# Optimization experiments

Hardware: AMD Instinct MI355X
Metric: run time of the kernel (lower is better)

## Reference

```python
import jax, jax.numpy as jnp
import numpy as np

N_NODES = 100000
N_EDGES = 1600000
IN_CH = 64
HID = 128
OUT_CH = 2
N_GRAPHS = 512
LN_EPS = 1e-5


def setup_inputs() -> dict:
    key = jax.random.key(0)
    ks = jax.random.split(key, 16)
    x = jax.random.normal(ks[0], (N_NODES, IN_CH), dtype=jnp.float32)
    edge_index = jax.random.randint(ks[1], (2, N_EDGES), 0, N_NODES, dtype=jnp.int64)
    batch = jnp.sort(jax.random.randint(ks[2], (N_NODES,), 0, N_GRAPHS, dtype=jnp.int64))

    def lin(k, fan_in, fan_out):
        bound = 1.0 / np.sqrt(fan_in)
        return jax.random.uniform(k, (fan_in, fan_out), jnp.float32, -bound, bound)

    inp = {"x": x, "edge_index": edge_index, "batch": batch}
    # SAGEConv 0: in->hid; SAGEConv 1,2: hid->hid
    inp["Wl0"] = lin(ks[3], IN_CH, HID); inp["bl0"] = jnp.zeros((HID,), jnp.float32)
    inp["Wr0"] = lin(ks[4], IN_CH, HID)
    inp["Wl1"] = lin(ks[5], HID, HID); inp["bl1"] = jnp.zeros((HID,), jnp.float32)
    inp["Wr1"] = lin(ks[6], HID, HID)
    inp["Wl2"] = lin(ks[7], HID, HID); inp["bl2"] = jnp.zeros((HID,), jnp.float32)
    inp["Wr2"] = lin(ks[8], HID, HID)
    # decode: LayerNorm(hid) + Linear(hid, out)
    inp["ln_g"] = jnp.ones((HID,), jnp.float32)
    inp["ln_b"] = jnp.zeros((HID,), jnp.float32)
    inp["Wd"] = lin(ks[9], HID, OUT_CH)
    inp["bd"] = jnp.zeros((OUT_CH,), jnp.float32)
    return inp


def _sage_conv(x, src, dst, Wl, bl, Wr):
    # mean aggregation of source features onto destination nodes
    s = jax.ops.segment_sum(x[src], dst, num_segments=N_NODES)  # [N, F]
    cnt = jax.ops.segment_sum(jnp.ones((src.shape[0],), x.dtype), dst, num_segments=N_NODES)
    agg = s / jnp.maximum(cnt, 1.0)[:, None]
    return agg @ Wl + bl + x @ Wr


def reference(x, edge_index, batch, Wl0, bl0, Wr0, Wl1, bl1, Wr1, Wl2, bl2, Wr2, ln_g, ln_b, Wd, bd):
    src, dst = edge_index[0], edge_index[1]
    h = jax.nn.relu(_sage_conv(x, src, dst, Wl0, bl0, Wr0))
    h = jax.nn.relu(_sage_conv(h, src, dst, Wl1, bl1, Wr1))
    h = jax.nn.relu(_sage_conv(h, src, dst, Wl2, bl2, Wr2))
    # global_add_pool
    g = jax.ops.segment_sum(h, batch, num_segments=N_GRAPHS)  # [G, HID]
    # decode: LayerNorm + Linear
    mu = jnp.mean(g, axis=-1, keepdims=True)
    var = jnp.mean(jnp.square(g - mu), axis=-1, keepdims=True)
    gn = (g - mu) * jax.lax.rsqrt(var + LN_EPS) * ln_g + ln_b
    return gn @ Wd + bd
```

## Files before the change

kernel.cpp:

```cpp
#include <hip/hip_runtime.h>

#define N_NODES  100000
#define N_EDGES  1600000
#define N_GRAPHS 512
#define LN_EPS   1e-5f

#define NB    256
#define NPB   391
#define BCAP  8192
#define PCHUNK 8192
#define PBLOCKS ((N_EDGES + PCHUNK - 1) / PCHUNK)
#define POOL_CHUNK 64
#define POOL_BLOCKS ((N_NODES + POOL_CHUNK - 1) / POOL_CHUNK)

typedef unsigned short u16;
typedef unsigned int   u32;
typedef __attribute__((ext_vector_type(8))) short bf16x8;
typedef __attribute__((ext_vector_type(4))) float f32x4;

__device__ __forceinline__ float b2f(u16 v) {
    u32 u = ((u32)v) << 16;
    return __builtin_bit_cast(float, u);
}
__device__ __forceinline__ u16 f2b(float f) {
    u32 u = __builtin_bit_cast(u32, f);
    u32 r = (u + 0x7fffu + ((u >> 16) & 1u)) >> 16;
    return (u16)r;
}


__global__ __launch_bounds__(256)
void partition_edges(const int* __restrict__ src, const int* __restrict__ dst,
                     int* __restrict__ bcnt, uint2* __restrict__ bpool) {
    __shared__ int hist[NB];
    __shared__ int gbase[NB];
    __shared__ int cur[NB];
    int t = threadIdx.x;
    int e0 = blockIdx.x * PCHUNK;
    int e1 = e0 + PCHUNK; if (e1 > N_EDGES) e1 = N_EDGES;

    hist[t] = 0;
    __syncthreads();
    for (int e = e0 + t; e < e1; e += 256)
        atomicAdd(&hist[dst[e] / NPB], 1);
    __syncthreads();
    int h = hist[t];
    gbase[t] = (h > 0) ? atomicAdd(&bcnt[t], h) : 0;
    cur[t] = 0;
    __syncthreads();
    for (int e = e0 + t; e < e1; e += 256) {
        int d = dst[e], s = src[e];
        int b = d / NPB;
        int p = atomicAdd(&cur[b], 1);
        bpool[(size_t)b * BCAP + gbase[b] + p] = make_uint2((u32)d, (u32)s);
    }
}

__global__ void scan_buckets(const int* __restrict__ bcnt, int* __restrict__ bbase,
                             int* __restrict__ offsets) {
    __shared__ int sh[NB];
    int t = threadIdx.x;
    int v = bcnt[t];
    sh[t] = v; __syncthreads();
    for (int off = 1; off < NB; off <<= 1) {
        int add = (t >= off) ? sh[t - off] : 0;
        __syncthreads();
        sh[t] += add;
        __syncthreads();
    }
    bbase[t] = sh[t] - v;
    if (t == NB - 1) offsets[N_NODES] = sh[t];
}

__global__ __launch_bounds__(256)
void build_csr_bucket(const int* __restrict__ bcnt, const int* __restrict__ bbase,
                      const uint2* __restrict__ bpool,
                      int* __restrict__ offsets, int* __restrict__ csr) {
    __shared__ int sA[512];
    __shared__ int sB[512];
    __shared__ int csrL[BCAP];
    int b = blockIdx.x, t = threadIdx.x;
    int nlo = b * NPB;
    int NL = N_NODES - nlo; if (NL > NPB) NL = NPB;
    int count = bcnt[b], base = bbase[b];
    const uint2* pool = bpool + (size_t)b * BCAP;

    sA[t] = 0; sA[t + 256] = 0;
    __syncthreads();
    for (int i = t; i < count; i += 256)
        atomicAdd(&sA[(int)pool[i].x - nlo], 1);
    __syncthreads();
    int c0 = sA[t], c1 = sA[t + 256];

    int* a = sA; int* c = sB;
    for (int off = 1; off < 512; off <<= 1) {
        c[t]       = a[t]       + ((t >= off)       ? a[t - off]       : 0);
        c[t + 256] = a[t + 256] + ((t + 256 >= off) ? a[t + 256 - off] : 0);
        __syncthreads();
        int* tmp = a; a = c; c = tmp;
    }
    int ex0 = a[t] - c0, ex1 = a[t + 256] - c1;
    if (t < NL)       offsets[nlo + t]       = base + ex0;
    if (t + 256 < NL) offsets[nlo + t + 256] = base + ex1;
    c[t] = ex0; c[t + 256] = ex1;
    __syncthreads();
    for (int i = t; i < count; i += 256) {
        uint2 p = pool[i];
        int pos = atomicAdd(&c[(int)p.x - nlo], 1);
        csrL[pos] = (int)p.y;
    }
    __syncthreads();
    for (int i = t; i < count; i += 256)
        csr[base + i] = csrL[i];
}


__global__ __launch_bounds__(256)
void conv_f32_bf16(const float* __restrict__ in, u16* __restrict__ out, int n4) {
    int i = blockIdx.x * 256 + threadIdx.x;
    if (i < n4) {
        float4 v = ((const float4*)in)[i];
        u32 lo = (u32)f2b(v.x) | ((u32)f2b(v.y) << 16);
        u32 hi = (u32)f2b(v.z) | ((u32)f2b(v.w) << 16);
        ((uint2*)out)[i] = make_uint2(lo, hi);
    }
}

__global__ __launch_bounds__(256)
void conv_weights(const float* __restrict__ Wl, const float* __restrict__ Wr,
                  int K1, int KC, u16* __restrict__ Wt) {
    int idx = blockIdx.x * 256 + threadIdx.x;
    if (idx >= 128 * KC) return;
    int c = idx / KC, k = idx % KC;
    float v = (k < K1) ? Wl[k * 128 + c] : Wr[(k - K1) * 128 + c];
    Wt[idx] = f2b(v);
}


template<int F>
__global__ __launch_bounds__(256)
void aggregate_bf16(const u16* __restrict__ in, const int* __restrict__ offsets,
                    const int* __restrict__ csr, u16* __restrict__ out) {
    int grp = threadIdx.x >> 5;
    int sub = threadIdx.x & 31;
    int n = blockIdx.x * 8 + grp;
    int o0 = offsets[n], o1 = offsets[n + 1];
    int d = o1 - o0;
    float inv = 1.0f / (float)(d > 1 ? d : 1);

    if (F == 128) {
        const uint2* base = (const uint2*)in;
        float acc[4][4];
        #pragma unroll
        for (int j = 0; j < 4; j++)
            #pragma unroll
            for (int c = 0; c < 4; c++) acc[j][c] = 0.f;

        int o = o0;
        for (; o + 4 <= o1; o += 4) {
            int s0 = csr[o + 0], s1 = csr[o + 1], s2 = csr[o + 2], s3 = csr[o + 3];
            uint2 v0 = base[(size_t)s0 * 32 + sub];
            uint2 v1 = base[(size_t)s1 * 32 + sub];
            uint2 v2 = base[(size_t)s2 * 32 + sub];
            uint2 v3 = base[(size_t)s3 * 32 + sub];
            acc[0][0] += b2f((u16)(v0.x & 0xffffu)); acc[0][1] += b2f((u16)(v0.x >> 16));
            acc[0][2] += b2f((u16)(v0.y & 0xffffu)); acc[0][3] += b2f((u16)(v0.y >> 16));
            acc[1][0] += b2f((u16)(v1.x & 0xffffu)); acc[1][1] += b2f((u16)(v1.x >> 16));
            acc[1][2] += b2f((u16)(v1.y & 0xffffu)); acc[1][3] += b2f((u16)(v1.y >> 16));
            acc[2][0] += b2f((u16)(v2.x & 0xffffu)); acc[2][1] += b2f((u16)(v2.x >> 16));
            acc[2][2] += b2f((u16)(v2.y & 0xffffu)); acc[2][3] += b2f((u16)(v2.y >> 16));
            acc[3][0] += b2f((u16)(v3.x & 0xffffu)); acc[3][1] += b2f((u16)(v3.x >> 16));
            acc[3][2] += b2f((u16)(v3.y & 0xffffu)); acc[3][3] += b2f((u16)(v3.y >> 16));
        }
        for (; o < o1; o++) {
            int s = csr[o];
            uint2 v = base[(size_t)s * 32 + sub];
            acc[0][0] += b2f((u16)(v.x & 0xffffu)); acc[0][1] += b2f((u16)(v.x >> 16));
            acc[0][2] += b2f((u16)(v.y & 0xffffu)); acc[0][3] += b2f((u16)(v.y >> 16));
        }
        float r0 = ((acc[0][0] + acc[1][0]) + (acc[2][0] + acc[3][0])) * inv;
        float r1 = ((acc[0][1] + acc[1][1]) + (acc[2][1] + acc[3][1])) * inv;
        float r2 = ((acc[0][2] + acc[1][2]) + (acc[2][2] + acc[3][2])) * inv;
        float r3 = ((acc[0][3] + acc[1][3]) + (acc[2][3] + acc[3][3])) * inv;
        uint2 w;
        w.x = (u32)f2b(r0) | ((u32)f2b(r1) << 16);
        w.y = (u32)f2b(r2) | ((u32)f2b(r3) << 16);
        ((uint2*)out)[(size_t)n * 32 + sub] = w;
    } else {
        const u32* base = (const u32*)in;
        float acc[4][2];
        #pragma unroll
        for (int j = 0; j < 4; j++) { acc[j][0] = 0.f; acc[j][1] = 0.f; }

        int o = o0;
        for (; o + 4 <= o1; o += 4) {
            int s0 = csr[o + 0], s1 = csr[o + 1], s2 = csr[o + 2], s3 = csr[o + 3];
            u32 v0 = base[(size_t)s0 * 32 + sub];
            u32 v1 = base[(size_t)s1 * 32 + sub];
            u32 v2 = base[(size_t)s2 * 32 + sub];
            u32 v3 = base[(size_t)s3 * 32 + sub];
            acc[0][0] += b2f((u16)(v0 & 0xffffu)); acc[0][1] += b2f((u16)(v0 >> 16));
            acc[1][0] += b2f((u16)(v1 & 0xffffu)); acc[1][1] += b2f((u16)(v1 >> 16));
            acc[2][0] += b2f((u16)(v2 & 0xffffu)); acc[2][1] += b2f((u16)(v2 >> 16));
            acc[3][0] += b2f((u16)(v3 & 0xffffu)); acc[3][1] += b2f((u16)(v3 >> 16));
        }
        for (; o < o1; o++) {
            int s = csr[o];
            u32 v = base[(size_t)s * 32 + sub];
            acc[0][0] += b2f((u16)(v & 0xffffu)); acc[0][1] += b2f((u16)(v >> 16));
        }
        float r0 = ((acc[0][0] + acc[1][0]) + (acc[2][0] + acc[3][0])) * inv;
        float r1 = ((acc[0][1] + acc[1][1]) + (acc[2][1] + acc[3][1])) * inv;
        ((u32*)out)[(size_t)n * 32 + sub] = (u32)f2b(r0) | ((u32)f2b(r1) << 16);
    }
}


template<int KHALF>
__global__ __launch_bounds__(256)
void gemm_mfma(const u16* __restrict__ A1, const u16* __restrict__ A2,
               const u16* __restrict__ Wt, const float* __restrict__ bias,
               u16* __restrict__ out) {
    constexpr int KC  = 2 * KHALF;
    constexpr int NKS = KC / 32;

    int t = threadIdx.x;
    int lane = t & 63, w = t >> 6;
    int l15 = lane & 15, l4 = lane >> 4;
    int mbase = blockIdx.x * 64;

    bf16x8 bfr[2][NKS];
    #pragma unroll
    for (int ct = 0; ct < 2; ct++)
        #pragma unroll
        for (int ks = 0; ks < NKS; ks++) {
            int row = w * 32 + ct * 16 + l15;
            int kb  = ks * 32 + l4 * 8;
            bfr[ct][ks] = *reinterpret_cast<const bf16x8*>(Wt + row * KC + kb);
        }

    f32x4 acc[4][2];
    #pragma unroll
    for (int i = 0; i < 4; i++)
        #pragma unroll
        for (int j = 0; j < 2; j++)
            acc[i][j] = (f32x4){0.f, 0.f, 0.f, 0.f};

    const bf16x8 zfr = {0, 0, 0, 0, 0, 0, 0, 0};

    #pragma unroll
    for (int ks = 0; ks < NKS; ks++) {
        const u16* Ab = (ks < NKS / 2) ? A1 : A2;
        int kb = (ks < NKS / 2) ? (ks * 32 + l4 * 8) : ((ks - NKS / 2) * 32 + l4 * 8);
        bf16x8 afr[4];
        #pragma unroll
        for (int rt = 0; rt < 4; rt++) {
            int row = mbase + rt * 16 + l15;
            afr[rt] = (row < N_NODES)
                ? *reinterpret_cast<const bf16x8*>(Ab + (size_t)row * KHALF + kb)
                : zfr;
        }
        #pragma unroll
        for (int rt = 0; rt < 4; rt++)
            #pragma unroll
            for (int ct = 0; ct < 2; ct++)
                acc[rt][ct] = __builtin_amdgcn_mfma_f32_16x16x32_bf16(
                    afr[rt], bfr[ct][ks], acc[rt][ct], 0, 0, 0);
    }

    #pragma unroll
    for (int ct = 0; ct < 2; ct++) {
        int col = w * 32 + ct * 16 + l15;
        float bv = bias[col];
        #pragma unroll
        for (int rt = 0; rt < 4; rt++) {
            #pragma unroll
            for (int j = 0; j < 4; j++) {
                int row = mbase + rt * 16 + l4 * 4 + j;
                if (row < N_NODES) {
                    float v = fmaxf(acc[rt][ct][j] + bv, 0.f);
                    out[(size_t)row * 128 + col] = f2b(v);
                }
            }
        }
    }
}


__global__ __launch_bounds__(128)
void pool_partial(const u16* __restrict__ h, const int* __restrict__ batch,
                  float* __restrict__ gpool) {
    int c = threadIdx.x;
    int n0 = blockIdx.x * POOL_CHUNK;
    int n1 = n0 + POOL_CHUNK; if (n1 > N_NODES) n1 = N_NODES;
    float run = 0.f;
    int curg = -1;
    for (int r = n0; r < n1; r++) {
        int gid = batch[r];
        if (gid != curg) {
            if (curg >= 0) atomicAdd(&gpool[curg * 128 + c], run);
            run = 0.f; curg = gid;
        }
        run += b2f(h[(size_t)r * 128 + c]);
    }
    if (curg >= 0) atomicAdd(&gpool[curg * 128 + c], run);
}

__global__ __launch_bounds__(64)
void ln_decode(const float* __restrict__ gpool,
               const float* __restrict__ ln_g, const float* __restrict__ ln_b,
               const float* __restrict__ Wd, const float* __restrict__ bd,
               float* __restrict__ out) {
    int g = blockIdx.x, lane = threadIdx.x;
    float v0 = gpool[g * 128 + lane];
    float v1 = gpool[g * 128 + 64 + lane];
    float s = v0 + v1;
    #pragma unroll
    for (int off = 32; off > 0; off >>= 1) s += __shfl_xor(s, off, 64);
    float mu = s * (1.0f / 128.f);
    float d0 = v0 - mu, d1 = v1 - mu;
    float q = d0 * d0 + d1 * d1;
    #pragma unroll
    for (int off = 32; off > 0; off >>= 1) q += __shfl_xor(q, off, 64);
    float rs = rsqrtf(q * (1.0f / 128.f) + LN_EPS);
    float gn0 = d0 * rs * ln_g[lane]      + ln_b[lane];
    float gn1 = d1 * rs * ln_g[64 + lane] + ln_b[64 + lane];
    float o0 = gn0 * Wd[lane * 2 + 0] + gn1 * Wd[(64 + lane) * 2 + 0];
    float o1 = gn0 * Wd[lane * 2 + 1] + gn1 * Wd[(64 + lane) * 2 + 1];
    #pragma unroll
    for (int off = 32; off > 0; off >>= 1) {
        o0 += __shfl_xor(o0, off, 64);
        o1 += __shfl_xor(o1, off, 64);
    }
    if (lane == 0) {
        out[g * 2 + 0] = o0 + bd[0];
        out[g * 2 + 1] = o1 + bd[1];
    }
}


extern "C" void kernel_launch(void* const* d_in, const int* in_sizes, int n_in,
                              void* d_out, int out_size, void* d_ws, size_t ws_size,
                              hipStream_t stream) {
    (void)in_sizes; (void)n_in; (void)out_size; (void)ws_size;

    const float* x     = (const float*)d_in[0];
    const int*   ei    = (const int*)d_in[1];
    const int*   batch = (const int*)d_in[2];
    const float* Wl0 = (const float*)d_in[3];
    const float* bl0 = (const float*)d_in[4];
    const float* Wr0 = (const float*)d_in[5];
    const float* Wl1 = (const float*)d_in[6];
    const float* bl1 = (const float*)d_in[7];
    const float* Wr1 = (const float*)d_in[8];
    const float* Wl2 = (const float*)d_in[9];
    const float* bl2 = (const float*)d_in[10];
    const float* Wr2 = (const float*)d_in[11];
    const float* ln_g = (const float*)d_in[12];
    const float* ln_b = (const float*)d_in[13];
    const float* Wd  = (const float*)d_in[14];
    const float* bd  = (const float*)d_in[15];
    float* out = (float*)d_out;

    const int* src = ei;
    const int* dst = ei + N_EDGES;

    char* ws = (char*)d_ws;
    int*   csr     = (int*)(ws + 0);
    int*   offsets = (int*)(ws + 6400000);
    int*   bcnt    = (int*)(ws + 6800128);
    int*   bbase   = (int*)(ws + 6801152);
    uint2* bpool   = (uint2*)(ws + 6802176);
    u16*   x16     = (u16*)(ws + 23579392);
    u16*   aggbuf  = (u16*)(ws + 36379392);
    u16*   bufB    = (u16*)(ws + 61979392);
    u16*   bufC    = (u16*)(ws + 87579392);
    u16*   Wt0     = (u16*)(ws + 113179392);
    u16*   Wt1     = (u16*)(ws + 113212160);
    u16*   Wt2     = (u16*)(ws + 113277696);
    float* gpool   = (float*)(ws + 113343232);

    hipMemsetAsync(bcnt, 0, NB * sizeof(int), stream);
    hipMemsetAsync(gpool, 0, N_GRAPHS * 128 * sizeof(float), stream);

    partition_edges<<<PBLOCKS, 256, 0, stream>>>(src, dst, bcnt, bpool);
    scan_buckets<<<1, 256, 0, stream>>>(bcnt, bbase, offsets);
    build_csr_bucket<<<NB, 256, 0, stream>>>(bcnt, bbase, bpool, offsets, csr);

    conv_f32_bf16<<<(N_NODES * 64 / 4 + 255) / 256, 256, 0, stream>>>(x, x16, N_NODES * 64 / 4);
    conv_weights<<<(128 * 128 + 255) / 256, 256, 0, stream>>>(Wl0, Wr0, 64, 128, Wt0);
    conv_weights<<<(128 * 256 + 255) / 256, 256, 0, stream>>>(Wl1, Wr1, 128, 256, Wt1);
    conv_weights<<<(128 * 256 + 255) / 256, 256, 0, stream>>>(Wl2, Wr2, 128, 256, Wt2);

    const int aggGrid  = N_NODES / 8;
    const int gemmGrid = (N_NODES + 63) / 64;

    aggregate_bf16<64><<<aggGrid, 256, 0, stream>>>(x16, offsets, csr, aggbuf);
    gemm_mfma<64><<<gemmGrid, 256, 0, stream>>>(aggbuf, x16, Wt0, bl0, bufB);
    aggregate_bf16<128><<<aggGrid, 256, 0, stream>>>(bufB, offsets, csr, aggbuf);
    gemm_mfma<128><<<gemmGrid, 256, 0, stream>>>(aggbuf, bufB, Wt1, bl1, bufC);
    aggregate_bf16<128><<<aggGrid, 256, 0, stream>>>(bufC, offsets, csr, aggbuf);
    gemm_mfma<128><<<gemmGrid, 256, 0, stream>>>(aggbuf, bufC, Wt2, bl2, bufB);

    pool_partial<<<POOL_BLOCKS, 128, 0, stream>>>(bufB, batch, gpool);
    ln_decode<<<N_GRAPHS, 64, 0, stream>>>(gpool, ln_g, ln_b, Wd, bd, out);
}
```

Measured before the change: 375.4 us.

## Split neighbor aggregation into column slices for better cache locality

Replaces the per-node full-row aggregation kernel with a sliced one. Each block handles 32 nodes but only one 8-u32 (32-byte) column slice of the feature row, with blocks ordered slice-major within each chunk. The aim is to shrink the per-pass working set of gathered rows so random neighbor gathers hit L2/MALL more often. It also adds nontemporal loads for the CSR and nontemporal stores for the output. The cost is that CSR indices and offsets are read once per slice (4x or 8x), each gather moves only 32 bytes per row segment, and there are many more blocks.

```diff
diff --git a/kernel.cpp b/kernel.cpp
--- a/kernel.cpp
+++ b/kernel.cpp
@@ -137,82 +137,48 @@
 }
 
 
-template<int F>
-__global__ __launch_bounds__(256)
-void aggregate_bf16(const u16* __restrict__ in, const int* __restrict__ offsets,
-                    const int* __restrict__ csr, u16* __restrict__ out) {
-    int grp = threadIdx.x >> 5;
-    int sub = threadIdx.x & 31;
-    int n = blockIdx.x * 8 + grp;
+template<int ROWU32, int SLICES>
+__global__ __launch_bounds__(256)
+void aggregate_slice(const u16* __restrict__ in, const int* __restrict__ offsets,
+                     const int* __restrict__ csr, u16* __restrict__ out) {
+    int slice = blockIdx.x & (SLICES - 1);
+    int chunk = blockIdx.x / SLICES;
+    int grp = threadIdx.x >> 3;
+    int sub = threadIdx.x & 7;
+    int n = chunk * 32 + grp;
     int o0 = offsets[n], o1 = offsets[n + 1];
-    int d = o1 - o0;
-    float inv = 1.0f / (float)(d > 1 ? d : 1);
-
-    if (F == 128) {
-        const uint2* base = (const uint2*)in;
-        float acc[4][4];
-        #pragma unroll
-        for (int j = 0; j < 4; j++)
-            #pragma unroll
-            for (int c = 0; c < 4; c++) acc[j][c] = 0.f;
-
-        int o = o0;
-        for (; o + 4 <= o1; o += 4) {
-            int s0 = csr[o + 0], s1 = csr[o + 1], s2 = csr[o + 2], s3 = csr[o + 3];
-            uint2 v0 = base[(size_t)s0 * 32 + sub];
-            uint2 v1 = base[(size_t)s1 * 32 + sub];
-            uint2 v2 = base[(size_t)s2 * 32 + sub];
-            uint2 v3 = base[(size_t)s3 * 32 + sub];
-            acc[0][0] += b2f((u16)(v0.x & 0xffffu)); acc[0][1] += b2f((u16)(v0.x >> 16));
-            acc[0][2] += b2f((u16)(v0.y & 0xffffu)); acc[0][3] += b2f((u16)(v0.y >> 16));
-            acc[1][0] += b2f((u16)(v1.x & 0xffffu)); acc[1][1] += b2f((u16)(v1.x >> 16));
-            acc[1][2] += b2f((u16)(v1.y & 0xffffu)); acc[1][3] += b2f((u16)(v1.y >> 16));
-            acc[2][0] += b2f((u16)(v2.x & 0xffffu)); acc[2][1] += b2f((u16)(v2.x >> 16));
-            acc[2][2] += b2f((u16)(v2.y & 0xffffu)); acc[2][3] += b2f((u16)(v2.y >> 16));
-            acc[3][0] += b2f((u16)(v3.x & 0xffffu)); acc[3][1] += b2f((u16)(v3.x >> 16));
-            acc[3][2] += b2f((u16)(v3.y & 0xffffu)); acc[3][3] += b2f((u16)(v3.y >> 16));
-        }
-        for (; o < o1; o++) {
-            int s = csr[o];
-            uint2 v = base[(size_t)s * 32 + sub];
-            acc[0][0] += b2f((u16)(v.x & 0xffffu)); acc[0][1] += b2f((u16)(v.x >> 16));
-            acc[0][2] += b2f((u16)(v.y & 0xffffu)); acc[0][3] += b2f((u16)(v.y >> 16));
-        }
-        float r0 = ((acc[0][0] + acc[1][0]) + (acc[2][0] + acc[3][0])) * inv;
-        float r1 = ((acc[0][1] + acc[1][1]) + (acc[2][1] + acc[3][1])) * inv;
-        float r2 = ((acc[0][2] + acc[1][2]) + (acc[2][2] + acc[3][2])) * inv;
-        float r3 = ((acc[0][3] + acc[1][3]) + (acc[2][3] + acc[3][3])) * inv;
-        uint2 w;
-        w.x = (u32)f2b(r0) | ((u32)f2b(r1) << 16);
-        w.y = (u32)f2b(r2) | ((u32)f2b(r3) << 16);
-        ((uint2*)out)[(size_t)n * 32 + sub] = w;
-    } else {
-        const u32* base = (const u32*)in;
-        float acc[4][2];
-        #pragma unroll
-        for (int j = 0; j < 4; j++) { acc[j][0] = 0.f; acc[j][1] = 0.f; }
-
-        int o = o0;
-        for (; o + 4 <= o1; o += 4) {
-            int s0 = csr[o + 0], s1 = csr[o + 1], s2 = csr[o + 2], s3 = csr[o + 3];
-            u32 v0 = base[(size_t)s0 * 32 + sub];
-            u32 v1 = base[(size_t)s1 * 32 + sub];
-            u32 v2 = base[(size_t)s2 * 32 + sub];
-            u32 v3 = base[(size_t)s3 * 32 + sub];
-            acc[0][0] += b2f((u16)(v0 & 0xffffu)); acc[0][1] += b2f((u16)(v0 >> 16));
-            acc[1][0] += b2f((u16)(v1 & 0xffffu)); acc[1][1] += b2f((u16)(v1 >> 16));
-            acc[2][0] += b2f((u16)(v2 & 0xffffu)); acc[2][1] += b2f((u16)(v2 >> 16));
-            acc[3][0] += b2f((u16)(v3 & 0xffffu)); acc[3][1] += b2f((u16)(v3 >> 16));
-        }
-        for (; o < o1; o++) {
-            int s = csr[o];
-            u32 v = base[(size_t)s * 32 + sub];
-            acc[0][0] += b2f((u16)(v & 0xffffu)); acc[0][1] += b2f((u16)(v >> 16));
-        }
-        float r0 = ((acc[0][0] + acc[1][0]) + (acc[2][0] + acc[3][0])) * inv;
-        float r1 = ((acc[0][1] + acc[1][1]) + (acc[2][1] + acc[3][1])) * inv;
-        ((u32*)out)[(size_t)n * 32 + sub] = (u32)f2b(r0) | ((u32)f2b(r1) << 16);
-    }
+    int deg = o1 - o0;
+    float inv = 1.0f / (float)(deg > 1 ? deg : 1);
+    const u32* base = (const u32*)in;
+    int coloff = slice * 8 + sub;
+
+    float a00 = 0.f, a01 = 0.f, a10 = 0.f, a11 = 0.f;
+    float a20 = 0.f, a21 = 0.f, a30 = 0.f, a31 = 0.f;
+
+    int o = o0;
+    for (; o + 4 <= o1; o += 4) {
+        int s0 = __builtin_nontemporal_load(&csr[o + 0]);
+        int s1 = __builtin_nontemporal_load(&csr[o + 1]);
+        int s2 = __builtin_nontemporal_load(&csr[o + 2]);
+        int s3 = __builtin_nontemporal_load(&csr[o + 3]);
+        u32 v0 = base[(size_t)s0 * ROWU32 + coloff];
+        u32 v1 = base[(size_t)s1 * ROWU32 + coloff];
+        u32 v2 = base[(size_t)s2 * ROWU32 + coloff];
+        u32 v3 = base[(size_t)s3 * ROWU32 + coloff];
+        a00 += b2f((u16)(v0 & 0xffffu)); a01 += b2f((u16)(v0 >> 16));
+        a10 += b2f((u16)(v1 & 0xffffu)); a11 += b2f((u16)(v1 >> 16));
+        a20 += b2f((u16)(v2 & 0xffffu)); a21 += b2f((u16)(v2 >> 16));
+        a30 += b2f((u16)(v3 & 0xffffu)); a31 += b2f((u16)(v3 >> 16));
+    }
+    for (; o < o1; o++) {
+        int s = __builtin_nontemporal_load(&csr[o]);
+        u32 v = base[(size_t)s * ROWU32 + coloff];
+        a00 += b2f((u16)(v & 0xffffu)); a01 += b2f((u16)(v >> 16));
+    }
+    float r0 = ((a00 + a10) + (a20 + a30)) * inv;
+    float r1 = ((a01 + a11) + (a21 + a31)) * inv;
+    u32 w = (u32)f2b(r0) | ((u32)f2b(r1) << 16);
+    __builtin_nontemporal_store(w, &((u32*)out)[(size_t)n * ROWU32 + coloff]);
 }
 
 
@@ -392,14 +358,15 @@
     conv_weights<<<(128 * 256 + 255) / 256, 256, 0, stream>>>(Wl1, Wr1, 128, 256, Wt1);
     conv_weights<<<(128 * 256 + 255) / 256, 256, 0, stream>>>(Wl2, Wr2, 128, 256, Wt2);
 
-    const int aggGrid  = N_NODES / 8;
-    const int gemmGrid = (N_NODES + 63) / 64;
-
-    aggregate_bf16<64><<<aggGrid, 256, 0, stream>>>(x16, offsets, csr, aggbuf);
+    const int agg128Grid = 8 * (N_NODES / 32);
+    const int agg64Grid  = 4 * (N_NODES / 32);
+    const int gemmGrid   = (N_NODES + 63) / 64;
+
+    aggregate_slice<32, 4><<<agg64Grid, 256, 0, stream>>>(x16, offsets, csr, aggbuf);
     gemm_mfma<64><<<gemmGrid, 256, 0, stream>>>(aggbuf, x16, Wt0, bl0, bufB);
-    aggregate_bf16<128><<<aggGrid, 256, 0, stream>>>(bufB, offsets, csr, aggbuf);
+    aggregate_slice<64, 8><<<agg128Grid, 256, 0, stream>>>(bufB, offsets, csr, aggbuf);
     gemm_mfma<128><<<gemmGrid, 256, 0, stream>>>(aggbuf, bufB, Wt1, bl1, bufC);
-    aggregate_bf16<128><<<aggGrid, 256, 0, stream>>>(bufC, offsets, csr, aggbuf);
+    aggregate_slice<64, 8><<<agg128Grid, 256, 0, stream>>>(bufC, offsets, csr, aggbuf);
     gemm_mfma<128><<<gemmGrid, 256, 0, stream>>>(aggbuf, bufC, Wt2, bl2, bufB);
 
     pool_partial<<<POOL_BLOCKS, 128, 0, stream>>>(bufB, batch, gpool);
```

After: 766.4 us. +104.2%, slower.
